# Performance work log

Hardware: AMD Instinct MI355X
Metric: run time of the kernel (lower is better)

The kernel has to match this reference:

```python
import jax, jax.numpy as jnp
import numpy as np

N_NODES = 100000
D = 256
HIDDEN = 256
E = 262144


def setup_inputs() -> dict:
    key = jax.random.key(0)
    ks = jax.random.split(key, 8)
    x_src = jax.random.normal(ks[0], (N_NODES, D), dtype=jnp.float32)
    x_dst = jax.random.normal(ks[1], (N_NODES, D), dtype=jnp.float32)
    # MLP params: Linear(in_src+in_dst -> hidden), ReLU, Linear(hidden -> 1)
    W1 = jax.random.normal(ks[2], (2 * D, HIDDEN), dtype=jnp.float32) * (1.0 / np.sqrt(2 * D))
    b1 = jnp.zeros((HIDDEN,), dtype=jnp.float32)
    W2 = jax.random.normal(ks[3], (HIDDEN, 1), dtype=jnp.float32) * (1.0 / np.sqrt(HIDDEN))
    b2 = jnp.zeros((1,), dtype=jnp.float32)
    edge_index = jax.random.randint(ks[4], (2, E), 0, N_NODES, dtype=jnp.int64)
    neg_edge_index = jax.random.randint(ks[5], (2, E), 0, N_NODES, dtype=jnp.int64)
    return {"x_src": x_src, "x_dst": x_dst, "W1": W1, "b1": b1, "W2": W2,
            "b2": b2, "edge_index": edge_index, "neg_edge_index": neg_edge_index}


def _score(xs, xd, W1, b1, W2, b2):
    # MLP scorer: cat -> Linear -> ReLU -> Linear -> squeeze
    h = jnp.concatenate([xs, xd], axis=-1) @ W1 + b1   # [E, HIDDEN]
    h = jax.nn.relu(h)
    return (h @ W2 + b2).squeeze(-1)                   # [E]


def reference(x_src, x_dst, W1, b1, W2, b2, edge_index, neg_edge_index):
    src, dst = edge_index[0], edge_index[1]
    nsrc, ndst = neg_edge_index[0], neg_edge_index[1]
    pos = _score(x_src[src], x_dst[dst], W1, b1, W2, b2)
    neg = _score(x_src[nsrc], x_dst[ndst], W1, b1, W2, b2)
    return pos, neg
```

## Files before the change

kernel.cpp:

```cpp
#include <hip/hip_runtime.h>

#define D_IN   256
#define HID    256
#define NNODES 100000
#define NEDGE  262144
#define NGROUPS 6250
#define GBLK   128
#define GW     16

typedef short short8            __attribute__((ext_vector_type(8)));
typedef float float4v           __attribute__((ext_vector_type(4)));
typedef unsigned short ushort8  __attribute__((ext_vector_type(8)));

__device__ __forceinline__ unsigned short f32_to_bf16_rne(float f) {
    unsigned int u = __float_as_uint(f);
    unsigned int r = u + 0x7FFFu + ((u >> 16) & 1u);
    return (unsigned short)(r >> 16);
}
__device__ __forceinline__ float bf16_to_f32(unsigned short h) {
    return __uint_as_float(((unsigned int)h) << 16);
}

__global__ __launch_bounds__(256) void convert_w(
    const float* __restrict__ W1, unsigned short* __restrict__ Wt)
{
    __shared__ float tile[64][65];
    const int z = blockIdx.z, kb = blockIdx.x * 64, nb = blockIdx.y * 64;
    const int t = threadIdx.x;
    const int g = t >> 6, c = t & 63;
#pragma unroll
    for (int r = 0; r < 16; r++) {
        int kl = g * 16 + r;
        tile[kl][c] = W1[((size_t)(z * 256 + kb + kl)) * 256 + nb + c];
    }
    __syncthreads();
#pragma unroll
    for (int r = 0; r < 16; r++) {
        int nl = g * 16 + r;
        Wt[((size_t)(z * 256 + nb + nl)) * 256 + kb + c] = f32_to_bf16_rne(tile[c][nl]);
    }
}

__global__ __launch_bounds__(1024, 4) void gemm_xw_mfma(
    const float* __restrict__ Xsrc, const float* __restrict__ Xdst,
    const unsigned short* __restrict__ Wt, const float* __restrict__ b1,
    unsigned short* __restrict__ U, unsigned short* __restrict__ V)
{
    const int zz = blockIdx.z;
    const float* X = zz ? Xdst : Xsrc;
    const unsigned short* Wz = Wt + (size_t)zz * 256 * 256;
    unsigned short* C = zz ? V : U;

    __shared__ __align__(16) unsigned short Bs[256 * 256];

    const int t = threadIdx.x;
#pragma unroll
    for (int i = 0; i < 8; i++) {
        int s = t + (i << 10);
        int n = s >> 5, c = s & 31;
        *(int4*)(Bs + n * 256 + ((c ^ (n & 7)) << 3)) =
            *(const int4*)(Wz + (size_t)n * 256 + (c << 3));
    }
    __syncthreads();

    const int w = t >> 6, lane = t & 63;
    const int quad = lane >> 4, l16 = lane & 15;
    const int r7 = l16 & 7;
    const unsigned short* Bl = Bs + l16 * 256;

    const int wid = w * GBLK + blockIdx.x;

    for (int g = wid; g < NGROUPS; g += GBLK * GW) {
        const int row = (g << 4) + l16;
        const float* Ap = X + (size_t)row * D_IN + (quad << 3);

        float4v acc[16];
#pragma unroll
        for (int i = 0; i < 16; i++) acc[i] = (float4v){0.f, 0.f, 0.f, 0.f};

        float4 a0 = *(const float4*)(Ap);
        float4 a1 = *(const float4*)(Ap + 4);

#pragma unroll 1
        for (int kk = 0; kk < 8; kk++) {
            float4 p0 = a0, p1 = a1;
            if (kk < 7) {
                p0 = *(const float4*)(Ap + (kk + 1) * 32);
                p1 = *(const float4*)(Ap + (kk + 1) * 32 + 4);
            }
            short8 af;
            af[0] = (short)f32_to_bf16_rne(a0.x);
            af[1] = (short)f32_to_bf16_rne(a0.y);
            af[2] = (short)f32_to_bf16_rne(a0.z);
            af[3] = (short)f32_to_bf16_rne(a0.w);
            af[4] = (short)f32_to_bf16_rne(a1.x);
            af[5] = (short)f32_to_bf16_rne(a1.y);
            af[6] = (short)f32_to_bf16_rne(a1.z);
            af[7] = (short)f32_to_bf16_rne(a1.w);

            const int cs = (((kk << 2) + quad) ^ r7) << 3;
#pragma unroll
            for (int tt = 0; tt < 16; tt++) {
                short8 bf = *(const short8*)(Bl + tt * 4096 + cs);
                acc[tt] = __builtin_amdgcn_mfma_f32_16x16x32_bf16(bf, af, acc[tt], 0, 0, 0);
            }
            a0 = p0; a1 = p1;
        }

        unsigned short* Crow = C + (size_t)row * HID + (quad << 2);
#pragma unroll
        for (int tt = 0; tt < 16; tt++) {
            float4v a = acc[tt];
            if (zz == 0) {
                float4 bb = *(const float4*)(b1 + tt * 16 + (quad << 2));
                a[0] += bb.x; a[1] += bb.y; a[2] += bb.z; a[3] += bb.w;
            }
            ushort4 pk;
            pk.x = f32_to_bf16_rne(a[0]);
            pk.y = f32_to_bf16_rne(a[1]);
            pk.z = f32_to_bf16_rne(a[2]);
            pk.w = f32_to_bf16_rne(a[3]);
            *(ushort4*)(Crow + tt * 16) = pk;
        }
    }
}

__global__ __launch_bounds__(256) void edge_score_bf16(
    const unsigned short* __restrict__ U, const unsigned short* __restrict__ V,
    const float* __restrict__ W2, const float* __restrict__ b2,
    const int* __restrict__ epos, const int* __restrict__ eneg,
    float* __restrict__ out)
{
    const int w = threadIdx.x >> 6, lane = threadIdx.x & 63;
    const int half = lane >> 5, hl = lane & 31;
    const int ebase = blockIdx.x * 64 + w * 16;

    const int* ei = (ebase < NEDGE) ? epos : eneg;
    const int eb2 = (ebase < NEDGE) ? ebase : ebase - NEDGE;

    int sidx[8], didx[8];
#pragma unroll
    for (int p = 0; p < 8; p++) {
        int e = eb2 + 2 * p + half;
        sidx[p] = ei[e];
        didx[p] = ei[NEDGE + e];
    }
    ushort8 uu[8], vv[8];
#pragma unroll
    for (int p = 0; p < 8; p++)
        uu[p] = *(const ushort8*)(U + (size_t)sidx[p] * HID + hl * 8);
#pragma unroll
    for (int p = 0; p < 8; p++)
        vv[p] = *(const ushort8*)(V + (size_t)didx[p] * HID + hl * 8);

    float w2r[8];
    *(float4*)&w2r[0] = *(const float4*)(W2 + hl * 8);
    *(float4*)&w2r[4] = *(const float4*)(W2 + hl * 8 + 4);
    const float bb2 = b2[0];

#pragma unroll
    for (int p = 0; p < 8; p++) {
        float s = 0.f;
#pragma unroll
        for (int q = 0; q < 8; q++)
            s += fmaxf(bf16_to_f32(uu[p][q]) + bf16_to_f32(vv[p][q]), 0.f) * w2r[q];
#pragma unroll
        for (int off = 16; off; off >>= 1)
            s += __shfl_xor(s, off, 64);
        if (hl == 0) out[ebase + 2 * p + half] = s + bb2;
    }
}

__global__ __launch_bounds__(256) void edge_score_direct(
    const float* __restrict__ xs_, const float* __restrict__ xd_,
    const float* __restrict__ W1, const float* __restrict__ b1,
    const float* __restrict__ W2, const float* __restrict__ b2,
    const int* __restrict__ epos, const int* __restrict__ eneg,
    float* __restrict__ out)
{
    __shared__ float xrow[2 * D_IN];
    __shared__ float red[256];
    const int e = blockIdx.x;
    const int* ei = (e < NEDGE) ? epos : eneg;
    const int e2  = (e < NEDGE) ? e : e - NEDGE;
    const int s = ei[e2];
    const int d = ei[NEDGE + e2];
    const int t = threadIdx.x;

    xrow[t]        = xs_[(size_t)s * D_IN + t];
    xrow[D_IN + t] = xd_[(size_t)d * D_IN + t];
    __syncthreads();

    float acc = b1[t];
    for (int k = 0; k < 2 * D_IN; k++)
        acc += xrow[k] * W1[(size_t)k * HID + t];
    acc = fmaxf(acc, 0.f);
    red[t] = acc * W2[t];
    __syncthreads();
    for (int st = 128; st; st >>= 1) {
        if (t < st) red[t] += red[t + st];
        __syncthreads();
    }
    if (t == 0) out[e] = red[0] + b2[0];
}

extern "C" void kernel_launch(void* const* d_in, const int* in_sizes, int n_in,
                              void* d_out, int out_size, void* d_ws, size_t ws_size,
                              hipStream_t stream) {
    const float* x_src = (const float*)d_in[0];
    const float* x_dst = (const float*)d_in[1];
    const float* W1    = (const float*)d_in[2];
    const float* b1    = (const float*)d_in[3];
    const float* W2    = (const float*)d_in[4];
    const float* b2    = (const float*)d_in[5];
    const int*   epos  = (const int*)d_in[6];
    const int*   eneg  = (const int*)d_in[7];
    float* out = (float*)d_out;

    const size_t uv   = (size_t)NNODES * HID;
    const size_t need = (2 * uv + 2 * 256 * 256) * sizeof(unsigned short);
    if (ws_size >= need) {
        unsigned short* U  = (unsigned short*)d_ws;
        unsigned short* V  = U + uv;
        unsigned short* Wt = V + uv;
        convert_w<<<dim3(4, 4, 2), 256, 0, stream>>>(W1, Wt);
        gemm_xw_mfma<<<dim3(GBLK, 1, 2), 1024, 0, stream>>>(x_src, x_dst, Wt, b1, U, V);
        edge_score_bf16<<<(2 * NEDGE) / 64, 256, 0, stream>>>(U, V, W2, b2, epos, eneg, out);
    } else {
        edge_score_direct<<<2 * NEDGE, 256, 0, stream>>>(x_src, x_dst, W1, b1, W2, b2, epos, eneg, out);
    }
}
```

Before: 326.4 us.

## Prefetch whole next A tile in registers and halve GEMM block size

Restructures the node-feature GEMM so each wave loads the full 16x256 fp32 A tile for its next group into registers while computing the current group, instead of prefetching one k-slice at a time. The block drops from 1024 to 512 threads (8 waves), and the launch bounds change to allow more registers per thread. This is meant to hide global-load latency behind the MFMA work. The cost is much higher register pressure (16 float4 plus 8 short8 per thread) and fewer waves per CU to hide latency, with the 128 KB LDS weight copy still limiting one block per CU.

```diff
diff --git a/kernel.cpp b/kernel.cpp
--- a/kernel.cpp
+++ b/kernel.cpp
@@ -6,7 +6,8 @@
 #define NEDGE  262144
 #define NGROUPS 6250
 #define GBLK   128
-#define GW     16
+#define GW     8
+#define GSTRIDE (GBLK * GW)
 
 typedef short short8            __attribute__((ext_vector_type(8)));
 typedef float float4v           __attribute__((ext_vector_type(4)));
@@ -41,7 +42,7 @@
     }
 }
 
-__global__ __launch_bounds__(1024, 4) void gemm_xw_mfma(
+__global__ __launch_bounds__(512, 2) void gemm_xw_mfma(
     const float* __restrict__ Xsrc, const float* __restrict__ Xdst,
     const unsigned short* __restrict__ Wt, const float* __restrict__ b1,
     unsigned short* __restrict__ U, unsigned short* __restrict__ V)
@@ -55,8 +56,8 @@
 
     const int t = threadIdx.x;
 #pragma unroll
-    for (int i = 0; i < 8; i++) {
-        int s = t + (i << 10);
+    for (int i = 0; i < 16; i++) {
+        int s = t + (i << 9);
         int n = s >> 5, c = s & 31;
         *(int4*)(Bs + n * 256 + ((c ^ (n & 7)) << 3)) =
             *(const int4*)(Wz + (size_t)n * 256 + (c << 3));
@@ -70,43 +71,53 @@
 
     const int wid = w * GBLK + blockIdx.x;
 
-    for (int g = wid; g < NGROUPS; g += GBLK * GW) {
-        const int row = (g << 4) + l16;
-        const float* Ap = X + (size_t)row * D_IN + (quad << 3);
-
+    float4 A[16];
+    int g = wid;
+    if (g < NGROUPS) {
+        const float* Ap = X + ((size_t)((g << 4) + l16)) * D_IN + (quad << 3);
+#pragma unroll
+        for (int kk = 0; kk < 8; kk++) {
+            A[2 * kk]     = *(const float4*)(Ap + kk * 32);
+            A[2 * kk + 1] = *(const float4*)(Ap + kk * 32 + 4);
+        }
+    }
+
+    for (; g < NGROUPS; g += GSTRIDE) {
+        short8 af[8];
+#pragma unroll
+        for (int kk = 0; kk < 8; kk++) {
+            float4 a0 = A[2 * kk], a1 = A[2 * kk + 1];
+            af[kk][0] = (short)f32_to_bf16_rne(a0.x);
+            af[kk][1] = (short)f32_to_bf16_rne(a0.y);
+            af[kk][2] = (short)f32_to_bf16_rne(a0.z);
+            af[kk][3] = (short)f32_to_bf16_rne(a0.w);
+            af[kk][4] = (short)f32_to_bf16_rne(a1.x);
+            af[kk][5] = (short)f32_to_bf16_rne(a1.y);
+            af[kk][6] = (short)f32_to_bf16_rne(a1.z);
+            af[kk][7] = (short)f32_to_bf16_rne(a1.w);
+        }
+        const int gn = g + GSTRIDE;
+        if (gn < NGROUPS) {
+            const float* Ap = X + ((size_t)((gn << 4) + l16)) * D_IN + (quad << 3);
+#pragma unroll
+            for (int kk = 0; kk < 8; kk++) {
+                A[2 * kk]     = *(const float4*)(Ap + kk * 32);
+                A[2 * kk + 1] = *(const float4*)(Ap + kk * 32 + 4);
+            }
+        }
         float4v acc[16];
 #pragma unroll
         for (int i = 0; i < 16; i++) acc[i] = (float4v){0.f, 0.f, 0.f, 0.f};
-
-        float4 a0 = *(const float4*)(Ap);
-        float4 a1 = *(const float4*)(Ap + 4);
-
-#pragma unroll 1
+#pragma unroll
         for (int kk = 0; kk < 8; kk++) {
-            float4 p0 = a0, p1 = a1;
-            if (kk < 7) {
-                p0 = *(const float4*)(Ap + (kk + 1) * 32);
-                p1 = *(const float4*)(Ap + (kk + 1) * 32 + 4);
-            }
-            short8 af;
-            af[0] = (short)f32_to_bf16_rne(a0.x);
-            af[1] = (short)f32_to_bf16_rne(a0.y);
-            af[2] = (short)f32_to_bf16_rne(a0.z);
-            af[3] = (short)f32_to_bf16_rne(a0.w);
-            af[4] = (short)f32_to_bf16_rne(a1.x);
-            af[5] = (short)f32_to_bf16_rne(a1.y);
-            af[6] = (short)f32_to_bf16_rne(a1.z);
-            af[7] = (short)f32_to_bf16_rne(a1.w);
-
             const int cs = (((kk << 2) + quad) ^ r7) << 3;
 #pragma unroll
             for (int tt = 0; tt < 16; tt++) {
                 short8 bf = *(const short8*)(Bl + tt * 4096 + cs);
-                acc[tt] = __builtin_amdgcn_mfma_f32_16x16x32_bf16(bf, af, acc[tt], 0, 0, 0);
+                acc[tt] = __builtin_amdgcn_mfma_f32_16x16x32_bf16(bf, af[kk], acc[tt], 0, 0, 0);
             }
-            a0 = p0; a1 = p1;
-        }
-
+        }
+        const int row = (g << 4) + l16;
         unsigned short* Crow = C + (size_t)row * HID + (quad << 2);
 #pragma unroll
         for (int tt = 0; tt < 16; tt++) {
@@ -224,7 +235,7 @@
         unsigned short* V  = U + uv;
         unsigned short* Wt = V + uv;
         convert_w<<<dim3(4, 4, 2), 256, 0, stream>>>(W1, Wt);
-        gemm_xw_mfma<<<dim3(GBLK, 1, 2), 1024, 0, stream>>>(x_src, x_dst, Wt, b1, U, V);
+        gemm_xw_mfma<<<dim3(GBLK, 1, 2), 512, 0, stream>>>(x_src, x_dst, Wt, b1, U, V);
         edge_score_bf16<<<(2 * NEDGE) / 64, 256, 0, stream>>>(U, V, W2, b2, epos, eneg, out);
     } else {
         edge_score_direct<<<2 * NEDGE, 256, 0, stream>>>(x_src, x_dst, W1, b1, W2, b2, epos, eneg, out);
```

Result: slower. 675.9 us (+107.1%).

## Deepen A-operand prefetch across groups and halve GEMM block size

Applied to the files above, without the earlier changes.

The node GEMM now keeps a 4-stage register ring of A fragments, prefetching four k-steps ahead and carrying loads across group iterations into the next group's rows. The k loop is fully unrolled. Blocks shrink from 1024 to 512 threads, which halves the waves per block, and launch bounds are relaxed to allow more registers per thread. The aim is to hide global-load latency from the streamed fp32 X rows. The cost is fewer waves to cover that latency and higher register pressure.

```diff
diff --git a/kernel.cpp b/kernel.cpp
--- a/kernel.cpp
+++ b/kernel.cpp
@@ -6,7 +6,8 @@
 #define NEDGE  262144
 #define NGROUPS 6250
 #define GBLK   128
-#define GW     16
+#define GW     8
+#define GSTRIDE (GBLK * GW)
 
 typedef short short8            __attribute__((ext_vector_type(8)));
 typedef float float4v           __attribute__((ext_vector_type(4)));
@@ -41,7 +42,7 @@
     }
 }
 
-__global__ __launch_bounds__(1024, 4) void gemm_xw_mfma(
+__global__ __launch_bounds__(512, 1) void gemm_xw_mfma(
     const float* __restrict__ Xsrc, const float* __restrict__ Xdst,
     const unsigned short* __restrict__ Wt, const float* __restrict__ b1,
     unsigned short* __restrict__ U, unsigned short* __restrict__ V)
@@ -55,8 +56,8 @@
 
     const int t = threadIdx.x;
 #pragma unroll
-    for (int i = 0; i < 8; i++) {
-        int s = t + (i << 10);
+    for (int i = 0; i < 16; i++) {
+        int s = t + (i << 9);
         int n = s >> 5, c = s & 31;
         *(int4*)(Bs + n * 256 + ((c ^ (n & 7)) << 3)) =
             *(const int4*)(Wz + (size_t)n * 256 + (c << 3));
@@ -70,24 +71,26 @@
 
     const int wid = w * GBLK + blockIdx.x;
 
-    for (int g = wid; g < NGROUPS; g += GBLK * GW) {
-        const int row = (g << 4) + l16;
-        const float* Ap = X + (size_t)row * D_IN + (quad << 3);
-
+    float4 P[8];
+    const float* ApCur = X + ((size_t)((wid << 4) + l16)) * D_IN + (quad << 3);
+    int gn = wid + GSTRIDE; if (gn >= NGROUPS) gn = wid;
+    const float* ApNext = X + ((size_t)((gn << 4) + l16)) * D_IN + (quad << 3);
+#pragma unroll
+    for (int s = 0; s < 4; s++) {
+        P[2 * s]     = *(const float4*)(ApCur + s * 32);
+        P[2 * s + 1] = *(const float4*)(ApCur + s * 32 + 4);
+    }
+
+#pragma unroll 1
+    for (int g = wid; g < NGROUPS; g += GSTRIDE) {
         float4v acc[16];
 #pragma unroll
         for (int i = 0; i < 16; i++) acc[i] = (float4v){0.f, 0.f, 0.f, 0.f};
 
-        float4 a0 = *(const float4*)(Ap);
-        float4 a1 = *(const float4*)(Ap + 4);
-
-#pragma unroll 1
+#pragma unroll
         for (int kk = 0; kk < 8; kk++) {
-            float4 p0 = a0, p1 = a1;
-            if (kk < 7) {
-                p0 = *(const float4*)(Ap + (kk + 1) * 32);
-                p1 = *(const float4*)(Ap + (kk + 1) * 32 + 4);
-            }
+            const int sl = kk & 3;
+            float4 a0 = P[2 * sl], a1 = P[2 * sl + 1];
             short8 af;
             af[0] = (short)f32_to_bf16_rne(a0.x);
             af[1] = (short)f32_to_bf16_rne(a0.y);
@@ -97,16 +100,19 @@
             af[5] = (short)f32_to_bf16_rne(a1.y);
             af[6] = (short)f32_to_bf16_rne(a1.z);
             af[7] = (short)f32_to_bf16_rne(a1.w);
-
+            const float* Lp = (kk < 4) ? (ApCur + (kk + 4) * 32)
+                                       : (ApNext + (kk - 4) * 32);
+            P[2 * sl]     = *(const float4*)(Lp);
+            P[2 * sl + 1] = *(const float4*)(Lp + 4);
             const int cs = (((kk << 2) + quad) ^ r7) << 3;
 #pragma unroll
             for (int tt = 0; tt < 16; tt++) {
                 short8 bf = *(const short8*)(Bl + tt * 4096 + cs);
                 acc[tt] = __builtin_amdgcn_mfma_f32_16x16x32_bf16(bf, af, acc[tt], 0, 0, 0);
             }
-            a0 = p0; a1 = p1;
         }
 
+        const int row = (g << 4) + l16;
         unsigned short* Crow = C + (size_t)row * HID + (quad << 2);
 #pragma unroll
         for (int tt = 0; tt < 16; tt++) {
@@ -122,6 +128,11 @@
             pk.w = f32_to_bf16_rne(a[3]);
             *(ushort4*)(Crow + tt * 16) = pk;
         }
+
+        ApCur = ApNext;
+        int g2 = g + 2 * GSTRIDE;
+        if (g2 >= NGROUPS) g2 = g;
+        ApNext = X + ((size_t)((g2 << 4) + l16)) * D_IN + (quad << 3);
     }
 }
 
@@ -224,7 +235,7 @@
         unsigned short* V  = U + uv;
         unsigned short* Wt = V + uv;
         convert_w<<<dim3(4, 4, 2), 256, 0, stream>>>(W1, Wt);
-        gemm_xw_mfma<<<dim3(GBLK, 1, 2), 1024, 0, stream>>>(x_src, x_dst, Wt, b1, U, V);
+        gemm_xw_mfma<<<dim3(GBLK, 1, 2), 512, 0, stream>>>(x_src, x_dst, Wt, b1, U, V);
         edge_score_bf16<<<(2 * NEDGE) / 64, 256, 0, stream>>>(U, V, W2, b2, epos, eneg, out);
     } else {
         edge_score_direct<<<2 * NEDGE, 256, 0, stream>>>(x_src, x_dst, W1, b1, W2, b2, epos, eneg, out);
```

Result: slower. 655.2 us (+100.7%).
